# Kernel optimization log

Measured on AMD Instinct MI355X. Metric: run time of the kernel, lower is better.

## Reference

```python
import jax, jax.numpy as jnp
import numpy as np

B, K, D = 4, 4096, 2048

def setup_inputs() -> dict:
    key = jax.random.key(0)
    k1, k2, k3 = jax.random.split(key, 3)
    x = jax.random.normal(k1, (B, K, D), dtype=jnp.float32)
    # Conv1d(dim, dim, kernel_size=1) weight [D, D, 1] squeezed to a dense [D_out, D_in] matrix
    W = jax.random.normal(k2, (D, D), dtype=jnp.float32) / np.sqrt(D)
    b = jax.random.normal(k3, (D,), dtype=jnp.float32) * 0.02
    return {"x": x, "W": W, "b": b}

def reference(x, W, b):
    # lam_t = sigmoid(dt_proj(u_t)); pointwise conv1d == per-timestep linear
    lam = jax.nn.sigmoid(jnp.einsum("bkd,ed->bke", x, W) + b)  # [B,K,D]
    # Gated linear recurrence: s_t = lam_t * s_{t-1} + (1 - lam_t) * u_t
    def step(s, inp):
        lam_t, u_t = inp  # each [B,D]
        s = lam_t * s + (1.0 - lam_t) * u_t
        return s, s
    s0 = jnp.zeros((x.shape[0], x.shape[2]), dtype=x.dtype)
    _, ys = jax.lax.scan(step, s0, (jnp.moveaxis(lam, 1, 0), jnp.moveaxis(x, 1, 0)))
    return jnp.moveaxis(ys, 0, 1)  # [B,K,D]
```

## Files before the change

### kernel.cpp

```cpp
#include <hip/hip_runtime.h>
#include <hip/hip_bf16.h>

#define B_SZ 4
#define K_SEQ 4096
#define D_DIM 2048
#define M_ROWS (B_SZ * K_SEQ)

#define BM 128
#define BN 128
#define BK 32

#define CHUNK 64
#define NCHUNK (K_SEQ / CHUNK)

typedef __attribute__((ext_vector_type(8))) short short8;
typedef __attribute__((ext_vector_type(4))) float floatx4;

__device__ __forceinline__ unsigned short f2bf_rne(float f) {
  unsigned int u = __float_as_uint(f);
  u += 0x7fffu + ((u >> 16) & 1u);
  return (unsigned short)(u >> 16);
}

__global__ void cvt_bf16_kernel(const float* __restrict__ in,
                                unsigned short* __restrict__ out, int n4) {
  int i = blockIdx.x * blockDim.x + threadIdx.x;
  if (i >= n4) return;
  float4 v = ((const float4*)in)[i];
  ushort4 o;
  o.x = f2bf_rne(v.x);
  o.y = f2bf_rne(v.y);
  o.z = f2bf_rne(v.z);
  o.w = f2bf_rne(v.w);
  ((ushort4*)out)[i] = o;
}

__device__ __forceinline__ void gl_lds16(const void* g, void* l) {
  __builtin_amdgcn_global_load_lds(
      (const __attribute__((address_space(1))) unsigned int*)g,
      (__attribute__((address_space(3))) unsigned int*)l, 16, 0, 0);
}

__global__ __launch_bounds__(256)
void gemm_lam_kernel(const unsigned short* __restrict__ A,
                     const unsigned short* __restrict__ Wb,
                     const float* __restrict__ bias,
                     float* __restrict__ lam) {
  __shared__ __align__(16) unsigned short As[BM * BK];
  __shared__ __align__(16) unsigned short Bs[BN * BK];

  const int tid = threadIdx.x;
  const int lane = tid & 63;
  const int wave = tid >> 6;
  const int bm = blockIdx.x * BM;
  const int bn = blockIdx.y * BN;
  const int wr = (wave >> 1) * 64;
  const int wc = (wave & 1) * 64;
  const int lrow = lane & 15;
  const int kgrp = lane >> 4;

  floatx4 acc[4][4];
#pragma unroll
  for (int i = 0; i < 4; ++i)
#pragma unroll
    for (int j = 0; j < 4; ++j)
      acc[i][j] = (floatx4){0.f, 0.f, 0.f, 0.f};

  const int c0 = tid, c1 = tid + 256;
  const unsigned short* gA0 = A + (size_t)(bm + (c0 >> 2)) * D_DIM + ((c0 & 3) << 3);
  const unsigned short* gA1 = A + (size_t)(bm + (c1 >> 2)) * D_DIM + ((c1 & 3) << 3);
  const unsigned short* gB0 = Wb + (size_t)(bn + (c0 >> 2)) * D_DIM + ((c0 & 3) << 3);
  const unsigned short* gB1 = Wb + (size_t)(bn + (c1 >> 2)) * D_DIM + ((c1 & 3) << 3);
  unsigned short* lA0 = As + c0 * 8;
  unsigned short* lA1 = As + c1 * 8;
  unsigned short* lB0 = Bs + c0 * 8;
  unsigned short* lB1 = Bs + c1 * 8;

  for (int k0 = 0; k0 < D_DIM; k0 += BK) {
    gl_lds16(gA0 + k0, lA0);
    gl_lds16(gA1 + k0, lA1);
    gl_lds16(gB0 + k0, lB0);
    gl_lds16(gB1 + k0, lB1);
    __syncthreads();

    short8 af[4], bf[4];
#pragma unroll
    for (int i = 0; i < 4; ++i) {
      af[i] = *(const short8*)(As + (wr + i * 16 + lrow) * BK + kgrp * 8);
      bf[i] = *(const short8*)(Bs + (wc + i * 16 + lrow) * BK + kgrp * 8);
    }
#pragma unroll
    for (int mi = 0; mi < 4; ++mi)
#pragma unroll
      for (int ni = 0; ni < 4; ++ni)
        acc[mi][ni] = __builtin_amdgcn_mfma_f32_16x16x32_bf16(
            af[mi], bf[ni], acc[mi][ni], 0, 0, 0);
    __syncthreads();
  }

  const int crow = (lane >> 4) << 2;
  const int ccol = lane & 15;
#pragma unroll
  for (int ni = 0; ni < 4; ++ni) {
    const int ge = bn + wc + ni * 16 + ccol;
    const float bb = bias[ge];
#pragma unroll
    for (int mi = 0; mi < 4; ++mi) {
      const int gm0 = bm + wr + mi * 16 + crow;
#pragma unroll
      for (int r = 0; r < 4; ++r) {
        float v = acc[mi][ni][r] + bb;
        lam[(size_t)(gm0 + r) * D_DIM + ge] = 1.0f / (1.0f + __expf(-v));
      }
    }
  }
}

__global__ void scan_reduce_kernel(const float* __restrict__ lam,
                                   const float* __restrict__ x,
                                   float* __restrict__ Ach,
                                   float* __restrict__ Bch) {
  int idx = blockIdx.x * blockDim.x + threadIdx.x;
  int d = idx & (D_DIM - 1);
  int c = (idx >> 11) & (NCHUNK - 1);
  int b = idx >> 17;
  size_t base = ((size_t)(b * K_SEQ + c * CHUNK)) * D_DIM + d;
  float Aacc = 1.f, Bv = 0.f;
#pragma unroll 8
  for (int t = 0; t < CHUNK; ++t) {
    size_t o = base + (size_t)t * D_DIM;
    float l = lam[o];
    float u = x[o];
    Aacc *= l;
    Bv = l * Bv + (1.f - l) * u;
  }
  Ach[idx] = Aacc;
  Bch[idx] = Bv;
}

__global__ void scan_prefix_kernel(const float* __restrict__ Ach,
                                   const float* __restrict__ Bch,
                                   float* __restrict__ Sst) {
  int idx = blockIdx.x * blockDim.x + threadIdx.x;
  int d = idx & (D_DIM - 1);
  int b = idx >> 11;
  float s = 0.f;
#pragma unroll 8
  for (int c = 0; c < NCHUNK; ++c) {
    int o = (b * NCHUNK + c) * D_DIM + d;
    Sst[o] = s;
    s = Ach[o] * s + Bch[o];
  }
}

__global__ void scan_apply_kernel(float* lamout, const float* __restrict__ x,
                                  const float* __restrict__ Sst) {
  int idx = blockIdx.x * blockDim.x + threadIdx.x;
  int d = idx & (D_DIM - 1);
  int c = (idx >> 11) & (NCHUNK - 1);
  int b = idx >> 17;
  size_t base = ((size_t)(b * K_SEQ + c * CHUNK)) * D_DIM + d;
  float s = Sst[idx];
#pragma unroll 8
  for (int t = 0; t < CHUNK; ++t) {
    size_t o = base + (size_t)t * D_DIM;
    float l = lamout[o];
    float u = x[o];
    s = l * s + (1.f - l) * u;
    lamout[o] = s;
  }
}

extern "C" void kernel_launch(void* const* d_in, const int* in_sizes, int n_in,
                              void* d_out, int out_size, void* d_ws, size_t ws_size,
                              hipStream_t stream) {
  const float* x = (const float*)d_in[0];
  const float* W = (const float*)d_in[1];
  const float* bias = (const float*)d_in[2];
  float* out = (float*)d_out;

  char* ws = (char*)d_ws;
  unsigned short* x_bf = (unsigned short*)ws;
  unsigned short* W_bf = (unsigned short*)(ws + (size_t)67108864);
  float* Ach = (float*)(ws + (size_t)75497472);
  float* Bch = (float*)(ws + (size_t)77594624);
  float* Sst = (float*)(ws + (size_t)79691776);

  {
    int n4 = M_ROWS * D_DIM / 4;
    cvt_bf16_kernel<<<n4 / 256, 256, 0, stream>>>(x, x_bf, n4);
  }
  {
    int n4 = D_DIM * D_DIM / 4;
    cvt_bf16_kernel<<<n4 / 256, 256, 0, stream>>>(W, W_bf, n4);
  }

  {
    dim3 grid(M_ROWS / BM, D_DIM / BN);
    gemm_lam_kernel<<<grid, 256, 0, stream>>>(x_bf, W_bf, bias, out);
  }

  {
    int total = B_SZ * NCHUNK * D_DIM;
    scan_reduce_kernel<<<total / 256, 256, 0, stream>>>(out, x, Ach, Bch);
    scan_prefix_kernel<<<(B_SZ * D_DIM) / 256, 256, 0, stream>>>(Ach, Bch, Sst);
    scan_apply_kernel<<<total / 256, 256, 0, stream>>>(out, x, Sst);
  }
}
```

Measured before the change: 538.1 us.

## Swizzle GEMM LDS layout, vectorize scan kernels, read bf16 x in scan

Applies an XOR swizzle to the LDS tile layout in the bf16 MFMA GEMM to reduce bank conflicts on fragment reads. The scan kernels now process four channels per thread with float4 loads and read the bf16 copy of x instead of fp32, cutting memory traffic. The two conversion launches are merged into one. Using bf16 x in the recurrence adds rounding error, and the vectorized scans launch four times fewer threads, which lowers occupancy.

```diff
diff --git a/kernel.cpp b/kernel.cpp
--- a/kernel.cpp
+++ b/kernel.cpp
@@ -21,18 +21,29 @@
   u += 0x7fffu + ((u >> 16) & 1u);
   return (unsigned short)(u >> 16);
 }
-
-__global__ void cvt_bf16_kernel(const float* __restrict__ in,
-                                unsigned short* __restrict__ out, int n4) {
+__device__ __forceinline__ float bf2f(unsigned short u) {
+  return __uint_as_float(((unsigned int)u) << 16);
+}
+
+#define NX4 (M_ROWS * D_DIM / 4)
+#define NW4 (D_DIM * D_DIM / 4)
+__global__ void cvt_bf16_kernel(const float* __restrict__ x,
+                                const float* __restrict__ W,
+                                unsigned short* __restrict__ xb,
+                                unsigned short* __restrict__ Wb) {
   int i = blockIdx.x * blockDim.x + threadIdx.x;
-  if (i >= n4) return;
-  float4 v = ((const float4*)in)[i];
+  const float* src;
+  unsigned short* dst;
+  int j;
+  if (i < NX4) { src = x; dst = xb; j = i; }
+  else         { src = W; dst = Wb; j = i - NX4; }
+  float4 v = ((const float4*)src)[j];
   ushort4 o;
   o.x = f2bf_rne(v.x);
   o.y = f2bf_rne(v.y);
   o.z = f2bf_rne(v.z);
   o.w = f2bf_rne(v.w);
-  ((ushort4*)out)[i] = o;
+  ((ushort4*)dst)[j] = o;
 }
 
 __device__ __forceinline__ void gl_lds16(const void* g, void* l) {
@@ -67,14 +78,18 @@
       acc[i][j] = (floatx4){0.f, 0.f, 0.f, 0.f};
 
   const int c0 = tid, c1 = tid + 256;
-  const unsigned short* gA0 = A + (size_t)(bm + (c0 >> 2)) * D_DIM + ((c0 & 3) << 3);
-  const unsigned short* gA1 = A + (size_t)(bm + (c1 >> 2)) * D_DIM + ((c1 & 3) << 3);
-  const unsigned short* gB0 = Wb + (size_t)(bn + (c0 >> 2)) * D_DIM + ((c0 & 3) << 3);
-  const unsigned short* gB1 = Wb + (size_t)(bn + (c1 >> 2)) * D_DIM + ((c1 & 3) << 3);
+  const int r0 = c0 >> 2, q0 = (c0 & 3) ^ ((r0 >> 1) & 3);
+  const int r1 = c1 >> 2, q1 = (c1 & 3) ^ ((r1 >> 1) & 3);
+  const unsigned short* gA0 = A + (size_t)(bm + r0) * D_DIM + (q0 << 3);
+  const unsigned short* gA1 = A + (size_t)(bm + r1) * D_DIM + (q1 << 3);
+  const unsigned short* gB0 = Wb + (size_t)(bn + r0) * D_DIM + (q0 << 3);
+  const unsigned short* gB1 = Wb + (size_t)(bn + r1) * D_DIM + (q1 << 3);
   unsigned short* lA0 = As + c0 * 8;
   unsigned short* lA1 = As + c1 * 8;
   unsigned short* lB0 = Bs + c0 * 8;
   unsigned short* lB1 = Bs + c1 * 8;
+
+  const int kq_s = kgrp ^ ((lrow >> 1) & 3);
 
   for (int k0 = 0; k0 < D_DIM; k0 += BK) {
     gl_lds16(gA0 + k0, lA0);
@@ -86,8 +101,10 @@
     short8 af[4], bf[4];
 #pragma unroll
     for (int i = 0; i < 4; ++i) {
-      af[i] = *(const short8*)(As + (wr + i * 16 + lrow) * BK + kgrp * 8);
-      bf[i] = *(const short8*)(Bs + (wc + i * 16 + lrow) * BK + kgrp * 8);
+      const int rowA = wr + i * 16 + lrow;
+      const int rowB = wc + i * 16 + lrow;
+      af[i] = *(const short8*)(As + rowA * 32 + kq_s * 8);
+      bf[i] = *(const short8*)(Bs + rowB * 32 + kq_s * 8);
     }
 #pragma unroll
     for (int mi = 0; mi < 4; ++mi)
@@ -117,57 +134,69 @@
 }
 
 __global__ void scan_reduce_kernel(const float* __restrict__ lam,
-                                   const float* __restrict__ x,
+                                   const unsigned short* __restrict__ xb,
                                    float* __restrict__ Ach,
                                    float* __restrict__ Bch) {
   int idx = blockIdx.x * blockDim.x + threadIdx.x;
-  int d = idx & (D_DIM - 1);
-  int c = (idx >> 11) & (NCHUNK - 1);
-  int b = idx >> 17;
-  size_t base = ((size_t)(b * K_SEQ + c * CHUNK)) * D_DIM + d;
-  float Aacc = 1.f, Bv = 0.f;
-#pragma unroll 8
+  int d4 = idx & (D_DIM / 4 - 1);
+  int c = (idx >> 9) & (NCHUNK - 1);
+  int b = idx >> 15;
+  size_t base = ((size_t)(b * K_SEQ + c * CHUNK)) * D_DIM + d4 * 4;
+  float4 Aacc = make_float4(1.f, 1.f, 1.f, 1.f);
+  float4 Bv = make_float4(0.f, 0.f, 0.f, 0.f);
+#pragma unroll 4
   for (int t = 0; t < CHUNK; ++t) {
     size_t o = base + (size_t)t * D_DIM;
-    float l = lam[o];
-    float u = x[o];
-    Aacc *= l;
-    Bv = l * Bv + (1.f - l) * u;
-  }
-  Ach[idx] = Aacc;
-  Bch[idx] = Bv;
+    float4 l = *(const float4*)(lam + o);
+    ushort4 ub = *(const ushort4*)(xb + o);
+    Aacc.x *= l.x; Bv.x = l.x * (Bv.x - bf2f(ub.x)) + bf2f(ub.x);
+    Aacc.y *= l.y; Bv.y = l.y * (Bv.y - bf2f(ub.y)) + bf2f(ub.y);
+    Aacc.z *= l.z; Bv.z = l.z * (Bv.z - bf2f(ub.z)) + bf2f(ub.z);
+    Aacc.w *= l.w; Bv.w = l.w * (Bv.w - bf2f(ub.w)) + bf2f(ub.w);
+  }
+  ((float4*)Ach)[idx] = Aacc;
+  ((float4*)Bch)[idx] = Bv;
 }
 
 __global__ void scan_prefix_kernel(const float* __restrict__ Ach,
                                    const float* __restrict__ Bch,
                                    float* __restrict__ Sst) {
   int idx = blockIdx.x * blockDim.x + threadIdx.x;
-  int d = idx & (D_DIM - 1);
-  int b = idx >> 11;
-  float s = 0.f;
-#pragma unroll 8
+  int d4 = idx & (D_DIM / 4 - 1);
+  int b = idx >> 9;
+  float4 s = make_float4(0.f, 0.f, 0.f, 0.f);
+#pragma unroll 4
   for (int c = 0; c < NCHUNK; ++c) {
-    int o = (b * NCHUNK + c) * D_DIM + d;
-    Sst[o] = s;
-    s = Ach[o] * s + Bch[o];
-  }
-}
-
-__global__ void scan_apply_kernel(float* lamout, const float* __restrict__ x,
+    int o4 = (b * NCHUNK + c) * (D_DIM / 4) + d4;
+    ((float4*)Sst)[o4] = s;
+    float4 A = ((const float4*)Ach)[o4];
+    float4 Bv = ((const float4*)Bch)[o4];
+    s.x = A.x * s.x + Bv.x;
+    s.y = A.y * s.y + Bv.y;
+    s.z = A.z * s.z + Bv.z;
+    s.w = A.w * s.w + Bv.w;
+  }
+}
+
+__global__ void scan_apply_kernel(float* lamout,
+                                  const unsigned short* __restrict__ xb,
                                   const float* __restrict__ Sst) {
   int idx = blockIdx.x * blockDim.x + threadIdx.x;
-  int d = idx & (D_DIM - 1);
-  int c = (idx >> 11) & (NCHUNK - 1);
-  int b = idx >> 17;
-  size_t base = ((size_t)(b * K_SEQ + c * CHUNK)) * D_DIM + d;
-  float s = Sst[idx];
-#pragma unroll 8
+  int d4 = idx & (D_DIM / 4 - 1);
+  int c = (idx >> 9) & (NCHUNK - 1);
+  int b = idx >> 15;
+  size_t base = ((size_t)(b * K_SEQ + c * CHUNK)) * D_DIM + d4 * 4;
+  float4 s = ((const float4*)Sst)[idx];
+#pragma unroll 4
   for (int t = 0; t < CHUNK; ++t) {
     size_t o = base + (size_t)t * D_DIM;
-    float l = lamout[o];
-    float u = x[o];
-    s = l * s + (1.f - l) * u;
-    lamout[o] = s;
+    float4 l = *(const float4*)(lamout + o);
+    ushort4 ub = *(const ushort4*)(xb + o);
+    s.x = l.x * (s.x - bf2f(ub.x)) + bf2f(ub.x);
+    s.y = l.y * (s.y - bf2f(ub.y)) + bf2f(ub.y);
+    s.z = l.z * (s.z - bf2f(ub.z)) + bf2f(ub.z);
+    s.w = l.w * (s.w - bf2f(ub.w)) + bf2f(ub.w);
+    *(float4*)(lamout + o) = s;
   }
 }
 
@@ -186,14 +215,7 @@
   float* Bch = (float*)(ws + (size_t)77594624);
   float* Sst = (float*)(ws + (size_t)79691776);
 
-  {
-    int n4 = M_ROWS * D_DIM / 4;
-    cvt_bf16_kernel<<<n4 / 256, 256, 0, stream>>>(x, x_bf, n4);
-  }
-  {
-    int n4 = D_DIM * D_DIM / 4;
-    cvt_bf16_kernel<<<n4 / 256, 256, 0, stream>>>(W, W_bf, n4);
-  }
+  cvt_bf16_kernel<<<(NX4 + NW4) / 256, 256, 0, stream>>>(x, W, x_bf, W_bf);
 
   {
     dim3 grid(M_ROWS / BM, D_DIM / BN);
@@ -201,9 +223,9 @@
   }
 
   {
-    int total = B_SZ * NCHUNK * D_DIM;
-    scan_reduce_kernel<<<total / 256, 256, 0, stream>>>(out, x, Ach, Bch);
-    scan_prefix_kernel<<<(B_SZ * D_DIM) / 256, 256, 0, stream>>>(Ach, Bch, Sst);
-    scan_apply_kernel<<<total / 256, 256, 0, stream>>>(out, x, Sst);
-  }
-}
+    int total4 = B_SZ * NCHUNK * D_DIM / 4;
+    scan_reduce_kernel<<<total4 / 256, 256, 0, stream>>>(out, x_bf, Ach, Bch);
+    scan_prefix_kernel<<<(B_SZ * D_DIM / 4) / 256, 256, 0, stream>>>(Ach, Bch, Sst);
+    scan_apply_kernel<<<total4 / 256, 256, 0, stream>>>(out, x_bf, Sst);
+  }
+}
```

Measured after the change: 484.9 us. 1.11x faster.
